# Performance work log

Hardware: AMD Instinct MI355X
Metric: run time of the kernel (lower is better)

The kernel has to match this reference:

```python
import jax, jax.numpy as jnp
import numpy as np
import math

B, S, D, H, MLP, L = 4, 1024, 512, 8, 2048, 4
C = D // H  # head dim = 64
K_RATIO = 0.25
TOPK = max(1, min(S, int(math.ceil(K_RATIO * S))))  # 256
EPS = 1e-6


def layernorm(x, w, b):
    mu = jnp.mean(x, axis=-1, keepdims=True)
    var = jnp.mean(jnp.square(x - mu), axis=-1, keepdims=True)
    return (x - mu) * jax.lax.rsqrt(var + EPS) * w + b


def dwconv3(x, w):
    # x: (B, Ch, S), w: (Ch, 1, 3) depthwise conv, padding 1
    return jax.lax.conv_general_dilated(
        x, w, window_strides=(1,), padding=[(1, 1)],
        dimension_numbers=('NCH', 'OIH', 'NCH'),
        feature_group_count=x.shape[1])


def setup_inputs() -> dict:
    key = jax.random.key(0)
    ks = jax.random.split(key, 16)
    g = lambda k, shape, s=0.02: jax.random.normal(k, shape, jnp.float32) * s
    return {
        'x': jax.random.normal(ks[0], (B, S, D), jnp.float32),
        'pos_emb': g(ks[1], (1, S, D)),
        'ln1_w': jnp.ones((L, D), jnp.float32),
        'ln1_b': jnp.zeros((L, D), jnp.float32),
        'qkv_w': g(ks[2], (L, 3 * D, D)),
        'dw_w': g(ks[3], (L, 3 * D, 1, 3), 0.1),
        'temp': jnp.ones((L, H), jnp.float32),
        'proj_w': g(ks[4], (L, D, D)),
        'ln2_w': jnp.ones((L, D), jnp.float32),
        'ln2_b': jnp.zeros((L, D), jnp.float32),
        'mlp_w1': g(ks[5], (L, MLP, D)),
        'mlp_b1': g(ks[6], (L, MLP), 1e-6),
        'mlp_w2': g(ks[7], (L, D, MLP)),
        'mlp_b2': g(ks[8], (L, D), 1e-6),
        'lnf_w': jnp.ones((D,), jnp.float32),
        'lnf_b': jnp.zeros((D,), jnp.float32),
    }


def _block(x, ln1_w, ln1_b, qkv_w, dw_w, temp, proj_w, ln2_w, ln2_b,
           mlp_w1, mlp_b1, mlp_w2, mlp_b2):
    # x: (B, S, D)
    h = layernorm(x, ln1_w, ln1_b).swapaxes(1, 2)        # (B, D, S)
    qkv = jnp.einsum('od,bds->bos', qkv_w, h)            # (B, 3D, S) 1x1 conv
    qkv = dwconv3(qkv, dw_w)                             # depthwise k=3
    q, k, v = jnp.split(qkv, 3, axis=1)                  # each (B, D, S)
    # 'b (head c) s -> b head s c'
    to_heads = lambda t: t.reshape(B, H, C, S).transpose(0, 1, 3, 2)
    q, k, v = to_heads(q), to_heads(k), to_heads(v)      # (B, H, S, C)
    q = q / jnp.maximum(jnp.linalg.norm(q, axis=-1, keepdims=True), 1e-12)
    k = k / jnp.maximum(jnp.linalg.norm(k, axis=-1, keepdims=True), 1e-12)
    scores = jnp.einsum('bhsc,bhtc->bhst', q, k) * temp[None, :, None, None]
    # top-k per query row: keep entries >= k-th largest, mask rest to -inf
    kth = jax.lax.top_k(scores, TOPK)[0][..., -1:]       # (B, H, S, 1)
    sparse = jnp.where(scores >= kth, scores, -jnp.inf)
    sparse = jnp.clip(sparse, -10000.0, 10000.0)         # -inf -> -10000
    attn = jax.nn.softmax(sparse, axis=-1)
    out = jnp.einsum('bhst,bhtc->bhsc', attn, v)         # (B, H, S, C)
    out = out.transpose(0, 1, 3, 2).reshape(B, D, S)     # 'b head s c -> b (head c) s'
    out = jnp.einsum('od,bds->bos', proj_w, out)         # project_out 1x1 conv
    x = x + out.swapaxes(1, 2)                           # residual (dropout=0)
    y = layernorm(x, ln2_w, ln2_b)
    y = jax.nn.gelu(y @ mlp_w1.T + mlp_b1, approximate=False) @ mlp_w2.T + mlp_b2
    return x + y


def reference(x, pos_emb, ln1_w, ln1_b, qkv_w, dw_w, temp, proj_w,
              ln2_w, ln2_b, mlp_w1, mlp_b1, mlp_w2, mlp_b2, lnf_w, lnf_b):
    h = x + pos_emb
    for i in range(L):
        h = _block(h, ln1_w[i], ln1_b[i], qkv_w[i], dw_w[i], temp[i], proj_w[i],
                   ln2_w[i], ln2_b[i], mlp_w1[i], mlp_b1[i], mlp_w2[i], mlp_b2[i])
    return layernorm(h, lnf_w, lnf_b)
```

## Files before the change

kernel.cpp:

```cpp
#include <hip/hip_runtime.h>

#define NB   4
#define SEQ  1024
#define DIM  512
#define NH   8
#define HD   64
#define MLPD 2048
#define NL   4
#define TOPKK 256
#define QKVD 1536
#define QT   16
#define SCB  1032

typedef short bh8 __attribute__((ext_vector_type(8)));
typedef float f32x4 __attribute__((ext_vector_type(4)));

__device__ __forceinline__ float b2f(unsigned short v) {
    return __uint_as_float(((unsigned)v) << 16);
}
__device__ __forceinline__ unsigned short f2b(float f) {
    unsigned u = __float_as_uint(f);
    u += 0x7FFFu + ((u >> 16) & 1u);
    return (unsigned short)(u >> 16);
}
__device__ __forceinline__ float ldin(const void* p, size_t i, int bf) {
    return bf ? b2f(((const unsigned short*)p)[i]) : ((const float*)p)[i];
}
__device__ __forceinline__ float wave_sum(float v) {
#pragma unroll
    for (int m = 32; m; m >>= 1) v += __shfl_xor(v, m);
    return v;
}
__device__ __forceinline__ unsigned f2key16(unsigned short u) {
    return (u & 0x8000u) ? (unsigned)((~u) & 0xFFFFu) : (unsigned)(u | 0x8000u);
}
__device__ __forceinline__ unsigned short key16b(unsigned k) {
    return (k & 0x8000u) ? (unsigned short)(k & 0x7FFFu)
                         : (unsigned short)((~k) & 0xFFFFu);
}
__device__ __forceinline__ uint4 pack8(const float* __restrict__ p) {
    uint4 r;
    r.x = (unsigned)f2b(p[0]) | ((unsigned)f2b(p[1]) << 16);
    r.y = (unsigned)f2b(p[2]) | ((unsigned)f2b(p[3]) << 16);
    r.z = (unsigned)f2b(p[4]) | ((unsigned)f2b(p[5]) << 16);
    r.w = (unsigned)f2b(p[6]) | ((unsigned)f2b(p[7]) << 16);
    return r;
}
__device__ __forceinline__ void async16(unsigned short* lds, const unsigned short* g) {
    __builtin_amdgcn_global_load_lds(
        (const __attribute__((address_space(1))) unsigned int*)g,
        (__attribute__((address_space(3))) unsigned int*)lds, 16, 0, 0);
}


__global__ void detect_kernel(const unsigned short* __restrict__ ln1w,
                              int* __restrict__ flag) {
    if (threadIdx.x == 0 && blockIdx.x == 0)
        *flag = (ln1w[0] == 0x3F80u) ? 1 : 0;
}

__global__ __launch_bounds__(256) void wcvt_kernel(
    const void* __restrict__ W, unsigned short* __restrict__ out,
    int n, const int* __restrict__ dflag) {
    int bf = *dflag;
    int idx = blockIdx.x * 256 + threadIdx.x;
    if (idx < n) out[idx] = f2b(ldin(W, idx, bf));
}

__global__ __launch_bounds__(256) void addpos_kernel(
    const void* __restrict__ x, const void* __restrict__ pos,
    float* __restrict__ h, const int* __restrict__ dflag) {
    int bf = *dflag;
    int idx = blockIdx.x * 256 + threadIdx.x;
    int sd = idx & (SEQ * DIM - 1);
    h[idx] = ldin(x, idx, bf) + ldin(pos, sd, bf);
}

__global__ __launch_bounds__(256) void ln_kernel(
    const float* __restrict__ in, const void* __restrict__ w,
    const void* __restrict__ bb, size_t wo, unsigned short* __restrict__ out,
    const int* __restrict__ dflag) {
    int bf = *dflag;
    __shared__ float red[4];
    int row = blockIdx.x, tid = threadIdx.x;
    int lane = tid & 63, wid = tid >> 6;
    const float* p = in + (size_t)row * DIM;
    float x0 = p[tid], x1 = p[tid + 256];
    float s = wave_sum(x0 + x1);
    if (!lane) red[wid] = s;
    __syncthreads();
    float mean = (red[0] + red[1] + red[2] + red[3]) * (1.0f / DIM);
    float d0 = x0 - mean, d1 = x1 - mean;
    float q = wave_sum(d0 * d0 + d1 * d1);
    __syncthreads();
    if (!lane) red[wid] = q;
    __syncthreads();
    float var = (red[0] + red[1] + red[2] + red[3]) * (1.0f / DIM);
    float rs = rsqrtf(var + 1e-6f);
    unsigned short* o = out + (size_t)row * DIM;
    o[tid]       = f2b(d0 * rs * ldin(w, wo + tid, bf) + ldin(bb, wo + tid, bf));
    o[tid + 256] = f2b(d1 * rs * ldin(w, wo + tid + 256, bf) + ldin(bb, wo + tid + 256, bf));
}

__global__ __launch_bounds__(256) void lnf_kernel(
    const float* __restrict__ in, const void* __restrict__ w,
    const void* __restrict__ bb, void* __restrict__ out,
    const int* __restrict__ dflag) {
    int bf = *dflag;
    __shared__ float red[4];
    int row = blockIdx.x, tid = threadIdx.x;
    int lane = tid & 63, wid = tid >> 6;
    const float* p = in + (size_t)row * DIM;
    float x0 = p[tid], x1 = p[tid + 256];
    float s = wave_sum(x0 + x1);
    if (!lane) red[wid] = s;
    __syncthreads();
    float mean = (red[0] + red[1] + red[2] + red[3]) * (1.0f / DIM);
    float d0 = x0 - mean, d1 = x1 - mean;
    float q = wave_sum(d0 * d0 + d1 * d1);
    __syncthreads();
    if (!lane) red[wid] = q;
    __syncthreads();
    float var = (red[0] + red[1] + red[2] + red[3]) * (1.0f / DIM);
    float rs = rsqrtf(var + 1e-6f);
    float v0 = d0 * rs * ldin(w, tid, bf) + ldin(bb, tid, bf);
    float v1 = d1 * rs * ldin(w, tid + 256, bf) + ldin(bb, tid + 256, bf);
    size_t o = (size_t)row * DIM;
    if (bf) {
        ((unsigned short*)out)[o + tid]       = f2b(v0);
        ((unsigned short*)out)[o + tid + 256] = f2b(v1);
    } else {
        ((float*)out)[o + tid]       = v0;
        ((float*)out)[o + tid + 256] = v1;
    }
}

__global__ __launch_bounds__(256) void gemm_mfma_kernel(
    const unsigned short* __restrict__ A, const void* __restrict__ W, size_t wo,
    const void* __restrict__ bias, size_t bo, void* __restrict__ C,
    int M, int N, int K, int flags, const int* __restrict__ dflag) {
    int bf = *dflag;
    __shared__ unsigned short As[128 * 32];
    __shared__ unsigned short Bs[128 * 32];
    int tid = threadIdx.x;
    int w = tid >> 6, l = tid & 63;
    int n0 = blockIdx.x * 128, m0 = blockIdx.y * 128;
    int wm = (w >> 1) * 64, wn = (w & 1) * 64;
    int lq = l & 15, lk = l >> 4;

    int srow = w * 32 + (l >> 2);
    int cb = (l & 3) * 8;
    const unsigned short* aG = A + (size_t)(m0 + srow) * K + cb;
    size_t wb = wo + (size_t)(n0 + srow) * K + cb;
    unsigned short* sA0 = &As[w * 1024 + l * 8];
    unsigned short* sA1 = &As[w * 1024 + 512 + l * 8];
    unsigned short* sB0 = &Bs[w * 1024 + l * 8];
    unsigned short* sB1 = &Bs[w * 1024 + 512 + l * 8];

    f32x4 acc[4][4];
#pragma unroll
    for (int i = 0; i < 4; ++i)
#pragma unroll
        for (int j = 0; j < 4; ++j)
            acc[i][j] = (f32x4){0.f, 0.f, 0.f, 0.f};

    for (int k0 = 0; k0 < K; k0 += 32) {
        uint4 a0 = *(const uint4*)(aG + k0);
        uint4 a1 = *(const uint4*)(aG + 16 * K + k0);
        uint4 b0, b1;
        if (bf) {
            b0 = *(const uint4*)((const unsigned short*)W + wb + k0);
            b1 = *(const uint4*)((const unsigned short*)W + wb + 16 * K + k0);
        } else {
            b0 = pack8((const float*)W + wb + k0);
            b1 = pack8((const float*)W + wb + 16 * K + k0);
        }
        __syncthreads();
        *(uint4*)sA0 = a0;
        *(uint4*)sA1 = a1;
        *(uint4*)sB0 = b0;
        *(uint4*)sB1 = b1;
        __syncthreads();
        bh8 af[4], bw[4];
#pragma unroll
        for (int i = 0; i < 4; ++i) {
            af[i] = *(const bh8*)&As[(wm + i * 16 + lq) * 32 + lk * 8];
            bw[i] = *(const bh8*)&Bs[(wn + i * 16 + lq) * 32 + lk * 8];
        }
#pragma unroll
        for (int i = 0; i < 4; ++i)
#pragma unroll
            for (int j = 0; j < 4; ++j)
                acc[i][j] = __builtin_amdgcn_mfma_f32_16x16x32_bf16(
                    af[i], bw[j], acc[i][j], 0, 0, 0);
    }

    int lr4 = lk * 4;
#pragma unroll
    for (int i = 0; i < 4; ++i) {
#pragma unroll
        for (int j = 0; j < 4; ++j) {
            int n = n0 + wn + j * 16 + lq;
            float bv = (flags & 4) ? ldin(bias, bo + n, bf) : 0.0f;
#pragma unroll
            for (int r = 0; r < 4; ++r) {
                int m = m0 + wm + i * 16 + lr4 + r;
                float v = acc[i][j][r] + bv;
                if (flags & 2) v = 0.5f * v * (1.0f + erff(v * 0.70710678118654752f));
                size_t o = (size_t)m * N + n;
                if (flags & 1) ((float*)C)[o] += v;
                else           ((unsigned short*)C)[o] = f2b(v);
            }
        }
    }
}

__global__ __launch_bounds__(256) void gemm_mfma_n64_kernel(
    const unsigned short* __restrict__ A, const void* __restrict__ W, size_t wo,
    const void* __restrict__ bias, size_t bo, void* __restrict__ C,
    int M, int N, int K, int flags, const int* __restrict__ dflag) {
    int bf = *dflag;
    __shared__ unsigned short As[128 * 32];
    __shared__ unsigned short Bs[64 * 32];
    int tid = threadIdx.x;
    int w = tid >> 6, l = tid & 63;
    int n0 = blockIdx.x * 64, m0 = blockIdx.y * 128;
    int wm = (w >> 1) * 64, wn = (w & 1) * 32;
    int lq = l & 15, lk = l >> 4;

    int srowA = w * 32 + (l >> 2);
    int cb = (l & 3) * 8;
    const unsigned short* aG = A + (size_t)(m0 + srowA) * K + cb;
    int srowB = w * 16 + (l >> 2);
    size_t wb = wo + (size_t)(n0 + srowB) * K + cb;
    unsigned short* sA0 = &As[w * 1024 + l * 8];
    unsigned short* sA1 = &As[w * 1024 + 512 + l * 8];
    unsigned short* sB0 = &Bs[w * 512 + l * 8];

    f32x4 acc[4][2];
#pragma unroll
    for (int i = 0; i < 4; ++i) {
        acc[i][0] = (f32x4){0.f, 0.f, 0.f, 0.f};
        acc[i][1] = (f32x4){0.f, 0.f, 0.f, 0.f};
    }

    for (int k0 = 0; k0 < K; k0 += 32) {
        uint4 a0 = *(const uint4*)(aG + k0);
        uint4 a1 = *(const uint4*)(aG + 16 * K + k0);
        uint4 b0;
        if (bf) b0 = *(const uint4*)((const unsigned short*)W + wb + k0);
        else    b0 = pack8((const float*)W + wb + k0);
        __syncthreads();
        *(uint4*)sA0 = a0;
        *(uint4*)sA1 = a1;
        *(uint4*)sB0 = b0;
        __syncthreads();
        bh8 af[4], bw[2];
#pragma unroll
        for (int i = 0; i < 4; ++i)
            af[i] = *(const bh8*)&As[(wm + i * 16 + lq) * 32 + lk * 8];
        bw[0] = *(const bh8*)&Bs[(wn + lq) * 32 + lk * 8];
        bw[1] = *(const bh8*)&Bs[(wn + 16 + lq) * 32 + lk * 8];
#pragma unroll
        for (int i = 0; i < 4; ++i) {
            acc[i][0] = __builtin_amdgcn_mfma_f32_16x16x32_bf16(af[i], bw[0], acc[i][0], 0, 0, 0);
            acc[i][1] = __builtin_amdgcn_mfma_f32_16x16x32_bf16(af[i], bw[1], acc[i][1], 0, 0, 0);
        }
    }

    int lr4 = lk * 4;
#pragma unroll
    for (int i = 0; i < 4; ++i) {
#pragma unroll
        for (int j = 0; j < 2; ++j) {
            int n = n0 + wn + j * 16 + lq;
            float bv = (flags & 4) ? ldin(bias, bo + n, bf) : 0.0f;
#pragma unroll
            for (int r = 0; r < 4; ++r) {
                int m = m0 + wm + i * 16 + lr4 + r;
                float v = acc[i][j][r] + bv;
                if (flags & 2) v = 0.5f * v * (1.0f + erff(v * 0.70710678118654752f));
                size_t o = (size_t)m * N + n;
                if (flags & 1) ((float*)C)[o] += v;
                else           ((unsigned short*)C)[o] = f2b(v);
            }
        }
    }
}

__global__ __launch_bounds__(256) void gemm_n64_dlds_kernel(
    const unsigned short* __restrict__ A, const unsigned short* __restrict__ W, size_t wo,
    const void* __restrict__ bias, size_t bo, void* __restrict__ C,
    int M, int N, int K, int flags, const int* __restrict__ dflag) {
    __shared__ unsigned short As[128 * 32];
    __shared__ unsigned short Bs[64 * 32];
    int tid = threadIdx.x;
    int w = tid >> 6, l = tid & 63;
    int n0 = blockIdx.x * 64, m0 = blockIdx.y * 128;
    int kz = blockIdx.z;
    int Ks = K / (int)gridDim.z;
    int kbeg = kz * Ks, kend = kbeg + Ks;
    int wm = (w >> 1) * 64, wn = (w & 1) * 32;
    int lq = l & 15, lk = l >> 4;

    int srowA = w * 32 + (l >> 2);
    int srowB = w * 16 + (l >> 2);
    int cb = (l & 3) * 8;
    const unsigned short* aG = A + (size_t)(m0 + srowA) * K + cb;
    const unsigned short* wG = W + wo + (size_t)(n0 + srowB) * K + cb;
    unsigned short* lA0 = As + w * 1024;
    unsigned short* lA1 = As + w * 1024 + 512;
    unsigned short* lB0 = Bs + w * 512;

    f32x4 acc[4][2];
#pragma unroll
    for (int i = 0; i < 4; ++i) {
        acc[i][0] = (f32x4){0.f, 0.f, 0.f, 0.f};
        acc[i][1] = (f32x4){0.f, 0.f, 0.f, 0.f};
    }

    for (int k0 = kbeg; k0 < kend; k0 += 32) {
        __syncthreads();
        async16(lA0, aG + k0);
        async16(lA1, aG + 16 * K + k0);
        async16(lB0, wG + k0);
        __syncthreads();
        bh8 af[4], bw[2];
#pragma unroll
        for (int i = 0; i < 4; ++i)
            af[i] = *(const bh8*)&As[(wm + i * 16 + lq) * 32 + lk * 8];
        bw[0] = *(const bh8*)&Bs[(wn + lq) * 32 + lk * 8];
        bw[1] = *(const bh8*)&Bs[(wn + 16 + lq) * 32 + lk * 8];
#pragma unroll
        for (int i = 0; i < 4; ++i) {
            acc[i][0] = __builtin_amdgcn_mfma_f32_16x16x32_bf16(af[i], bw[0], acc[i][0], 0, 0, 0);
            acc[i][1] = __builtin_amdgcn_mfma_f32_16x16x32_bf16(af[i], bw[1], acc[i][1], 0, 0, 0);
        }
    }

    int bf = (flags & 4) ? *dflag : 0;
    int lr4 = lk * 4;
#pragma unroll
    for (int i = 0; i < 4; ++i) {
#pragma unroll
        for (int j = 0; j < 2; ++j) {
            int n = n0 + wn + j * 16 + lq;
            float bv = ((flags & 4) && kz == 0) ? ldin(bias, bo + n, bf) : 0.0f;
#pragma unroll
            for (int r = 0; r < 4; ++r) {
                int m = m0 + wm + i * 16 + lr4 + r;
                float v = acc[i][j][r] + bv;
                if (flags & 2) v = 0.5f * v * (1.0f + erff(v * 0.70710678118654752f));
                size_t o = (size_t)m * N + n;
                if (flags & 8)      atomicAdd(&((float*)C)[o], v);
                else if (flags & 1) ((float*)C)[o] += v;
                else                ((unsigned short*)C)[o] = f2b(v);
            }
        }
    }
}

__global__ __launch_bounds__(256) void dwconv_kernel(
    const unsigned short* __restrict__ in, const void* __restrict__ w, size_t wo,
    unsigned short* __restrict__ out, const int* __restrict__ dflag) {
    int bf = *dflag;
    int idx = blockIdx.x * 256 + threadIdx.x;
    int o = idx % QKVD;
    int s = (idx / QKVD) & (SEQ - 1);
    float w0 = ldin(w, wo + o * 3 + 0, bf);
    float w1 = ldin(w, wo + o * 3 + 1, bf);
    float w2 = ldin(w, wo + o * 3 + 2, bf);
    float acc = w1 * b2f(in[idx]);
    if (s > 0)        acc += w0 * b2f(in[idx - QKVD]);
    if (s < SEQ - 1)  acc += w2 * b2f(in[idx + QKVD]);
    out[idx] = f2b(acc);
}

__global__ __launch_bounds__(256) void qkvprep_kernel(
    unsigned short* __restrict__ qkv, const void* __restrict__ temp, size_t to,
    unsigned short* __restrict__ Kc, unsigned short* __restrict__ Vt,
    const int* __restrict__ dflag) {
    int bf = *dflag;
    int tid = threadIdx.x;
    int g = tid >> 6, c = tid & 63;
    int gid = blockIdx.x * 4 + g;
    int h = gid & 7;
    int bs = gid >> 3;
    int s = bs & (SEQ - 1), b = bs >> 10;
    int bh = b * NH + h;
    unsigned short* p = qkv + (size_t)bs * QKVD + h * HD;
    float qv = b2f(p[c]), kv = b2f(p[512 + c]);
    float qs = wave_sum(qv * qv);
    float ks = wave_sum(kv * kv);
    float t = ldin(temp, to + h, bf);
    p[c] = f2b(qv / fmaxf(sqrtf(qs), 1e-12f) * t);
    Kc[((size_t)bh * SEQ + s) * HD + c] = f2b(kv / fmaxf(sqrtf(ks), 1e-12f));
    Vt[(((size_t)bh * 32 + (s >> 5)) * HD + c) * 32 + (s & 31)] = p[1024 + c];
}

__global__ __launch_bounds__(256) void attn_kernel(
    const unsigned short* __restrict__ qkv, const unsigned short* __restrict__ Kc,
    const unsigned short* __restrict__ Vt, unsigned short* __restrict__ outp) {
    __shared__ unsigned short sc16[QT * SCB];
    __shared__ unsigned hist[4][256];
    __shared__ float kth16[QT];
    __shared__ float inv16[QT];
    __shared__ float wmax[4][QT];
    __shared__ unsigned selB[4];
    __shared__ unsigned selK[4];

    int tid = threadIdx.x;
    int w = tid >> 6, l = tid & 63;
    int lq = l & 15, lk = l >> 4;
    int bid = blockIdx.x;
    int qt = bid & 63;
    int h = (bid >> 6) & 7;
    int b = bid >> 9;
    int bh = b * NH + h;

    const unsigned short* base = qkv + (size_t)b * SEQ * QKVD;

    const unsigned short* qp = base + (size_t)(qt * QT + lq) * QKVD + h * HD + lk * 8;
    bh8 aq0 = *(const bh8*)(qp);
    bh8 aq1 = *(const bh8*)(qp + 32);

    const unsigned short* Kbh = Kc + (size_t)bh * SEQ * HD;
    float vm0 = -3.0e38f, vm1 = -3.0e38f, vm2 = -3.0e38f, vm3 = -3.0e38f;
    for (int kb = 0; kb < 16; ++kb) {
        int key0 = (w * 16 + kb) * 16;
        const unsigned short* kp = Kbh + (size_t)(key0 + lq) * HD + lk * 8;
        bh8 b0 = *(const bh8*)(kp);
        bh8 b1 = *(const bh8*)(kp + 32);
        f32x4 acc = {0.f, 0.f, 0.f, 0.f};
        acc = __builtin_amdgcn_mfma_f32_16x16x32_bf16(aq0, b0, acc, 0, 0, 0);
        acc = __builtin_amdgcn_mfma_f32_16x16x32_bf16(aq1, b1, acc, 0, 0, 0);
        sc16[(lk * 4 + 0) * SCB + key0 + lq] = f2b(acc[0]);
        sc16[(lk * 4 + 1) * SCB + key0 + lq] = f2b(acc[1]);
        sc16[(lk * 4 + 2) * SCB + key0 + lq] = f2b(acc[2]);
        sc16[(lk * 4 + 3) * SCB + key0 + lq] = f2b(acc[3]);
        vm0 = fmaxf(vm0, acc[0]); vm1 = fmaxf(vm1, acc[1]);
        vm2 = fmaxf(vm2, acc[2]); vm3 = fmaxf(vm3, acc[3]);
    }
#pragma unroll
    for (int off = 1; off < 16; off <<= 1) {
        vm0 = fmaxf(vm0, __shfl_xor(vm0, off));
        vm1 = fmaxf(vm1, __shfl_xor(vm1, off));
        vm2 = fmaxf(vm2, __shfl_xor(vm2, off));
        vm3 = fmaxf(vm3, __shfl_xor(vm3, off));
    }
    if (lq == 0) {
        wmax[w][lk * 4 + 0] = b2f(f2b(vm0));
        wmax[w][lk * 4 + 1] = b2f(f2b(vm1));
        wmax[w][lk * 4 + 2] = b2f(f2b(vm2));
        wmax[w][lk * 4 + 3] = b2f(f2b(vm3));
    }
    __syncthreads();

    unsigned* histw = &hist[w][0];
    for (int rr = 0; rr < 4; ++rr) {
        int row = w * 4 + rr;
        unsigned keyv[16];
#pragma unroll
        for (int j = 0; j < 16; ++j)
            keyv[j] = f2key16(sc16[row * SCB + l + 64 * j]);
        unsigned kk = TOPKK;
        unsigned prefval = 0;
        for (int pass = 1; pass >= 0; --pass) {
            int shift = pass << 3;
            *(uint4*)&histw[l * 4] = (uint4){0u, 0u, 0u, 0u};
            __builtin_amdgcn_wave_barrier();
#pragma unroll
            for (int j = 0; j < 16; ++j) {
                unsigned kx = keyv[j];
                bool part = pass ? true : ((kx >> 8) == prefval);
                if (part) atomicAdd(&histw[(kx >> shift) & 0xFFu], 1u);
            }
            __builtin_amdgcn_wave_barrier();
            uint4 hv = *(uint4*)&histw[l * 4];
            unsigned h0 = hv.x, h1 = hv.y, h2 = hv.z, h3 = hv.w;
            unsigned tot = h0 + h1 + h2 + h3;
            unsigned incl = tot;
#pragma unroll
            for (int off = 1; off < 64; off <<= 1) {
                unsigned t = __shfl_down(incl, off);
                if (l + off < 64) incl += t;
            }
            unsigned T = incl - tot;
            unsigned s0 = T + tot, s1 = T + h1 + h2 + h3, s2 = T + h2 + h3, s3 = T + h3;
            if (s0 >= kk && s0 - h0 < kk) { selB[w] = (unsigned)(l * 4 + 0); selK[w] = kk - (s0 - h0); }
            if (s1 >= kk && s1 - h1 < kk) { selB[w] = (unsigned)(l * 4 + 1); selK[w] = kk - (s1 - h1); }
            if (s2 >= kk && s2 - h2 < kk) { selB[w] = (unsigned)(l * 4 + 2); selK[w] = kk - (s2 - h2); }
            if (s3 >= kk && s3 - h3 < kk) { selB[w] = (unsigned)(l * 4 + 3); selK[w] = kk - (s3 - h3); }
            __builtin_amdgcn_wave_barrier();
            prefval = pass ? selB[w] : ((prefval << 8) | selB[w]);
            kk = selK[w];
        }
        if (l == 0) kth16[row] = b2f(key16b(prefval));
    }

    {
        int row = tid >> 4, sub = tid & 15;
        float kth = kth16[row];
        float m = fmaxf(fmaxf(wmax[0][row], wmax[1][row]),
                        fmaxf(wmax[2][row], wmax[3][row]));
        m = fminf(fmaxf(m, -10000.f), 10000.f);
        unsigned short* srow = sc16 + row * SCB;
        float ssum = 0.f;
#pragma unroll
        for (int j = 0; j < 8; ++j) {
            uint4 v4 = *(uint4*)&srow[sub * 8 + 128 * j];
            unsigned short us[8] = {
                (unsigned short)(v4.x & 0xFFFFu), (unsigned short)(v4.x >> 16),
                (unsigned short)(v4.y & 0xFFFFu), (unsigned short)(v4.y >> 16),
                (unsigned short)(v4.z & 0xFFFFu), (unsigned short)(v4.z >> 16),
                (unsigned short)(v4.w & 0xFFFFu), (unsigned short)(v4.w >> 16)};
            unsigned short ps[8];
#pragma unroll
            for (int e = 0; e < 8; ++e) {
                float a = b2f(us[e]);
                a = (a >= kth) ? fminf(fmaxf(a, -10000.f), 10000.f) : -10000.f;
                float ev = expf(a - m);
                ssum += ev;
                ps[e] = f2b(ev);
            }
            uint4 o4;
            o4.x = (unsigned)ps[0] | ((unsigned)ps[1] << 16);
            o4.y = (unsigned)ps[2] | ((unsigned)ps[3] << 16);
            o4.z = (unsigned)ps[4] | ((unsigned)ps[5] << 16);
            o4.w = (unsigned)ps[6] | ((unsigned)ps[7] << 16);
            *(uint4*)&srow[sub * 8 + 128 * j] = o4;
        }
#pragma unroll
        for (int off = 1; off < 16; off <<= 1) ssum += __shfl_xor(ssum, off);
        if (sub == 0) inv16[row] = 1.0f / ssum;
    }
    __syncthreads();

    {
        const unsigned short* Vbh = Vt + (size_t)bh * SEQ * HD;
        const unsigned short* prow = sc16 + lq * SCB;
        f32x4 oacc = {0.f, 0.f, 0.f, 0.f};
        for (int tc = 0; tc < 32; ++tc) {
            bh8 ap = *(const bh8*)&prow[tc * 32 + lk * 8];
            bh8 bv = *(const bh8*)(Vbh + (size_t)tc * 2048 + (w * 16 + lq) * 32 + lk * 8);
            oacc = __builtin_amdgcn_mfma_f32_16x16x32_bf16(ap, bv, oacc, 0, 0, 0);
        }
#pragma unroll
        for (int r = 0; r < 4; ++r) {
            int q = lk * 4 + r;
            float val = oacc[r] * inv16[q];
            outp[((size_t)(b * SEQ + qt * QT + q)) * DIM + h * HD + w * 16 + lq] = f2b(val);
        }
    }
}

extern "C" void kernel_launch(void* const* d_in, const int* in_sizes, int n_in,
                              void* d_out, int out_size, void* d_ws, size_t ws_size,
                              hipStream_t stream) {
    (void)in_sizes; (void)n_in; (void)out_size;
    const void* x     = d_in[0];
    const void* pos   = d_in[1];
    const void* ln1w  = d_in[2];
    const void* ln1b  = d_in[3];
    const void* qkvw  = d_in[4];
    const void* dww   = d_in[5];
    const void* temp  = d_in[6];
    const void* projw = d_in[7];
    const void* ln2w  = d_in[8];
    const void* ln2b  = d_in[9];
    const void* w1    = d_in[10];
    const void* b1    = d_in[11];
    const void* w2    = d_in[12];
    const void* b2    = d_in[13];
    const void* lnfw  = d_in[14];
    const void* lnfb  = d_in[15];

    float* wsf = (float*)d_ws;
    const size_t M1 = (size_t)1024 * 1024;
    float*          h    = wsf;
    unsigned short* bn   = (unsigned short*)(wsf + 2 * M1);
    unsigned short* C2   = (unsigned short*)(wsf + 3 * M1);
    unsigned short* C1   = (unsigned short*)(wsf + 6 * M1);
    unsigned short* Vt   = (unsigned short*)(wsf + 6 * M1);
    unsigned short* Kc   = (unsigned short*)(wsf + 7 * M1);
    unsigned short* Mb   = C2;
    int*            flag = (int*)(wsf + 9 * M1);
    unsigned short* Wc   = (unsigned short*)(wsf + 9 * M1 + 16);

    const int MTOK  = NB * SEQ;
    const int nQKVW = NL * QKVD * DIM;
    const int nPROJ = NL * DIM * DIM;
    const int nW1   = NL * MLPD * DIM;
    const int nW2   = NL * DIM * MLPD;
    const size_t wcElems = (size_t)nQKVW + nPROJ + nW1 + nW2;
    const int big = ws_size >= ((9 * M1 + 16) * 4 + wcElems * 2);

    unsigned short* WcQ  = Wc;
    unsigned short* WcP  = Wc + nQKVW;
    unsigned short* WcW1 = Wc + nQKVW + nPROJ;
    unsigned short* WcW2 = Wc + nQKVW + nPROJ + (size_t)nW1;

    detect_kernel<<<1, 64, 0, stream>>>((const unsigned short*)ln1w, flag);
    addpos_kernel<<<(NB * SEQ * DIM) / 256, 256, 0, stream>>>(x, pos, h, flag);

    if (big) {
        wcvt_kernel<<<nQKVW / 256, 256, 0, stream>>>(qkvw, WcQ, nQKVW, flag);
        wcvt_kernel<<<nPROJ / 256, 256, 0, stream>>>(projw, WcP, nPROJ, flag);
        wcvt_kernel<<<nW1 / 256, 256, 0, stream>>>(w1, WcW1, nW1, flag);
        wcvt_kernel<<<nW2 / 256, 256, 0, stream>>>(w2, WcW2, nW2, flag);
    }

    for (int l = 0; l < NL; ++l) {
        ln_kernel<<<MTOK, 256, 0, stream>>>(h, ln1w, ln1b, (size_t)l * DIM, bn, flag);
        if (big) {
            gemm_n64_dlds_kernel<<<dim3(QKVD / 64, MTOK / 128, 1), 256, 0, stream>>>(
                bn, WcQ, (size_t)l * QKVD * DIM, nullptr, 0, C1,
                MTOK, QKVD, DIM, 0, flag);
        } else {
            gemm_mfma_kernel<<<dim3(QKVD / 128, MTOK / 128), 256, 0, stream>>>(
                bn, qkvw, (size_t)l * QKVD * DIM, nullptr, 0, C1,
                MTOK, QKVD, DIM, 0, flag);
        }
        dwconv_kernel<<<(NB * SEQ * QKVD) / 256, 256, 0, stream>>>(
            C1, dww, (size_t)l * QKVD * 3, C2, flag);
        qkvprep_kernel<<<(NB * SEQ * NH) / 4, 256, 0, stream>>>(
            C2, temp, (size_t)l * NH, Kc, Vt, flag);
        attn_kernel<<<NB * NH * (SEQ / QT), 256, 0, stream>>>(C2, Kc, Vt, bn);
        if (big) {
            gemm_n64_dlds_kernel<<<dim3(DIM / 64, MTOK / 128, 2), 256, 0, stream>>>(
                bn, WcP, (size_t)l * DIM * DIM, nullptr, 0, h,
                MTOK, DIM, DIM, 8, flag);
        } else {
            gemm_mfma_n64_kernel<<<dim3(DIM / 64, MTOK / 128), 256, 0, stream>>>(
                bn, projw, (size_t)l * DIM * DIM, nullptr, 0, h,
                MTOK, DIM, DIM, 1, flag);
        }
        ln_kernel<<<MTOK, 256, 0, stream>>>(h, ln2w, ln2b, (size_t)l * DIM, bn, flag);
        if (big) {
            gemm_n64_dlds_kernel<<<dim3(MLPD / 64, MTOK / 128, 1), 256, 0, stream>>>(
                bn, WcW1, (size_t)l * MLPD * DIM, b1, (size_t)l * MLPD, Mb,
                MTOK, MLPD, DIM, 2 | 4, flag);
            gemm_n64_dlds_kernel<<<dim3(DIM / 64, MTOK / 128, 2), 256, 0, stream>>>(
                Mb, WcW2, (size_t)l * DIM * MLPD, b2, (size_t)l * DIM, h,
                MTOK, DIM, MLPD, 8 | 4, flag);
        } else {
            gemm_mfma_kernel<<<dim3(MLPD / 128, MTOK / 128), 256, 0, stream>>>(
                bn, w1, (size_t)l * MLPD * DIM, b1, (size_t)l * MLPD, Mb,
                MTOK, MLPD, DIM, 2 | 4, flag);
            gemm_mfma_n64_kernel<<<dim3(DIM / 64, MTOK / 128), 256, 0, stream>>>(
                Mb, w2, (size_t)l * DIM * MLPD, b2, (size_t)l * DIM, h,
                MTOK, DIM, MLPD, 1 | 4, flag);
        }
    }

    lnf_kernel<<<MTOK, 256, 0, stream>>>(h, lnfw, lnfb, d_out, flag);
}
```

Measured before the change: 1.075 ms.

## Replace histogram radix top-k with ballot-based bitwise threshold search in attention

```diff
diff --git a/kernel.cpp b/kernel.cpp
--- a/kernel.cpp
+++ b/kernel.cpp
@@ -402,12 +402,7 @@
     const unsigned short* __restrict__ qkv, const unsigned short* __restrict__ Kc,
     const unsigned short* __restrict__ Vt, unsigned short* __restrict__ outp) {
     __shared__ unsigned short sc16[QT * SCB];
-    __shared__ unsigned hist[4][256];
-    __shared__ float kth16[QT];
     __shared__ float inv16[QT];
-    __shared__ float wmax[4][QT];
-    __shared__ unsigned selB[4];
-    __shared__ unsigned selK[4];
 
     int tid = threadIdx.x;
     int w = tid >> 6, l = tid & 63;
@@ -425,7 +420,6 @@
     bh8 aq1 = *(const bh8*)(qp + 32);
 
     const unsigned short* Kbh = Kc + (size_t)bh * SEQ * HD;
-    float vm0 = -3.0e38f, vm1 = -3.0e38f, vm2 = -3.0e38f, vm3 = -3.0e38f;
     for (int kb = 0; kb < 16; ++kb) {
         int key0 = (w * 16 + kb) * 16;
         const unsigned short* kp = Kbh + (size_t)(key0 + lq) * HD + lk * 8;
@@ -438,101 +432,59 @@
         sc16[(lk * 4 + 1) * SCB + key0 + lq] = f2b(acc[1]);
         sc16[(lk * 4 + 2) * SCB + key0 + lq] = f2b(acc[2]);
         sc16[(lk * 4 + 3) * SCB + key0 + lq] = f2b(acc[3]);
-        vm0 = fmaxf(vm0, acc[0]); vm1 = fmaxf(vm1, acc[1]);
-        vm2 = fmaxf(vm2, acc[2]); vm3 = fmaxf(vm3, acc[3]);
-    }
-#pragma unroll
-    for (int off = 1; off < 16; off <<= 1) {
-        vm0 = fmaxf(vm0, __shfl_xor(vm0, off));
-        vm1 = fmaxf(vm1, __shfl_xor(vm1, off));
-        vm2 = fmaxf(vm2, __shfl_xor(vm2, off));
-        vm3 = fmaxf(vm3, __shfl_xor(vm3, off));
-    }
-    if (lq == 0) {
-        wmax[w][lk * 4 + 0] = b2f(f2b(vm0));
-        wmax[w][lk * 4 + 1] = b2f(f2b(vm1));
-        wmax[w][lk * 4 + 2] = b2f(f2b(vm2));
-        wmax[w][lk * 4 + 3] = b2f(f2b(vm3));
-    }
-    __syncthreads();
-
-    unsigned* histw = &hist[w][0];
+    }
+    __syncthreads();
+
     for (int rr = 0; rr < 4; ++rr) {
         int row = w * 4 + rr;
-        unsigned keyv[16];
-#pragma unroll
-        for (int j = 0; j < 16; ++j)
-            keyv[j] = f2key16(sc16[row * SCB + l + 64 * j]);
-        unsigned kk = TOPKK;
-        unsigned prefval = 0;
-        for (int pass = 1; pass >= 0; --pass) {
-            int shift = pass << 3;
-            *(uint4*)&histw[l * 4] = (uint4){0u, 0u, 0u, 0u};
-            __builtin_amdgcn_wave_barrier();
-#pragma unroll
-            for (int j = 0; j < 16; ++j) {
-                unsigned kx = keyv[j];
-                bool part = pass ? true : ((kx >> 8) == prefval);
-                if (part) atomicAdd(&histw[(kx >> shift) & 0xFFu], 1u);
-            }
-            __builtin_amdgcn_wave_barrier();
-            uint4 hv = *(uint4*)&histw[l * 4];
-            unsigned h0 = hv.x, h1 = hv.y, h2 = hv.z, h3 = hv.w;
-            unsigned tot = h0 + h1 + h2 + h3;
-            unsigned incl = tot;
-#pragma unroll
-            for (int off = 1; off < 64; off <<= 1) {
-                unsigned t = __shfl_down(incl, off);
-                if (l + off < 64) incl += t;
-            }
-            unsigned T = incl - tot;
-            unsigned s0 = T + tot, s1 = T + h1 + h2 + h3, s2 = T + h2 + h3, s3 = T + h3;
-            if (s0 >= kk && s0 - h0 < kk) { selB[w] = (unsigned)(l * 4 + 0); selK[w] = kk - (s0 - h0); }
-            if (s1 >= kk && s1 - h1 < kk) { selB[w] = (unsigned)(l * 4 + 1); selK[w] = kk - (s1 - h1); }
-            if (s2 >= kk && s2 - h2 < kk) { selB[w] = (unsigned)(l * 4 + 2); selK[w] = kk - (s2 - h2); }
-            if (s3 >= kk && s3 - h3 < kk) { selB[w] = (unsigned)(l * 4 + 3); selK[w] = kk - (s3 - h3); }
-            __builtin_amdgcn_wave_barrier();
-            prefval = pass ? selB[w] : ((prefval << 8) | selB[w]);
-            kk = selK[w];
-        }
-        if (l == 0) kth16[row] = b2f(key16b(prefval));
-    }
-
-    {
-        int row = tid >> 4, sub = tid & 15;
-        float kth = kth16[row];
-        float m = fmaxf(fmaxf(wmax[0][row], wmax[1][row]),
-                        fmaxf(wmax[2][row], wmax[3][row]));
+        unsigned short* srow = sc16 + row * SCB;
+        uint4 r0 = *(const uint4*)&srow[l * 8];
+        uint4 r1 = *(const uint4*)&srow[512 + l * 8];
+        unsigned wd[8] = {r0.x, r0.y, r0.z, r0.w, r1.x, r1.y, r1.z, r1.w};
+        float v[16];
+#pragma unroll
+        for (int j = 0; j < 8; ++j) {
+            v[2 * j]     = __uint_as_float(wd[j] << 16);
+            v[2 * j + 1] = __uint_as_float(wd[j] & 0xFFFF0000u);
+        }
+        float m = v[0];
+#pragma unroll
+        for (int j = 1; j < 16; ++j) m = fmaxf(m, v[j]);
+#pragma unroll
+        for (int off = 1; off < 64; off <<= 1) m = fmaxf(m, __shfl_xor(m, off));
         m = fminf(fmaxf(m, -10000.f), 10000.f);
-        unsigned short* srow = sc16 + row * SCB;
+        unsigned T = 0;
+        for (int bit = 15; bit >= 0; --bit) {
+            unsigned cand = T | (1u << bit);
+            float tf = b2f(key16b(cand));
+            unsigned cnt = 0;
+#pragma unroll
+            for (int j = 0; j < 16; ++j)
+                cnt += (unsigned)__popcll(__ballot(v[j] >= tf));
+            if (cnt >= TOPKK) T = cand;
+        }
+        float kth = b2f(key16b(T));
+        float e[16];
         float ssum = 0.f;
 #pragma unroll
+        for (int j = 0; j < 16; ++j) {
+            float a = fminf(fmaxf(v[j], -10000.f), 10000.f);
+            float ev = (v[j] >= kth) ? __expf(a - m) : 0.0f;
+            ssum += ev;
+            e[j] = ev;
+        }
+#pragma unroll
+        for (int off = 1; off < 64; off <<= 1) ssum += __shfl_xor(ssum, off);
+        if (l == 0) inv16[row] = 1.0f / ssum;
+        unsigned pw[8];
+#pragma unroll
         for (int j = 0; j < 8; ++j) {
-            uint4 v4 = *(uint4*)&srow[sub * 8 + 128 * j];
-            unsigned short us[8] = {
-                (unsigned short)(v4.x & 0xFFFFu), (unsigned short)(v4.x >> 16),
-                (unsigned short)(v4.y & 0xFFFFu), (unsigned short)(v4.y >> 16),
-                (unsigned short)(v4.z & 0xFFFFu), (unsigned short)(v4.z >> 16),
-                (unsigned short)(v4.w & 0xFFFFu), (unsigned short)(v4.w >> 16)};
-            unsigned short ps[8];
-#pragma unroll
-            for (int e = 0; e < 8; ++e) {
-                float a = b2f(us[e]);
-                a = (a >= kth) ? fminf(fmaxf(a, -10000.f), 10000.f) : -10000.f;
-                float ev = expf(a - m);
-                ssum += ev;
-                ps[e] = f2b(ev);
-            }
-            uint4 o4;
-            o4.x = (unsigned)ps[0] | ((unsigned)ps[1] << 16);
-            o4.y = (unsigned)ps[2] | ((unsigned)ps[3] << 16);
-            o4.z = (unsigned)ps[4] | ((unsigned)ps[5] << 16);
-            o4.w = (unsigned)ps[6] | ((unsigned)ps[7] << 16);
-            *(uint4*)&srow[sub * 8 + 128 * j] = o4;
-        }
-#pragma unroll
-        for (int off = 1; off < 16; off <<= 1) ssum += __shfl_xor(ssum, off);
-        if (sub == 0) inv16[row] = 1.0f / ssum;
+            unsigned r;
+            asm("v_cvt_pk_bf16_f32 %0, %1, %2" : "=v"(r) : "v"(e[2 * j]), "v"(e[2 * j + 1]));
+            pw[j] = r;
+        }
+        *(uint4*)&srow[l * 8]       = (uint4){pw[0], pw[1], pw[2], pw[3]};
+        *(uint4*)&srow[512 + l * 8] = (uint4){pw[4], pw[5], pw[6], pw[7]};
     }
     __syncthreads();
 
```

Measured after the change: 1.045 ms. -2.8%, faster.
